# Performance work log

Measured on AMD Instinct MI355X. Metric: run time of the kernel, lower is better.

Reference implementation:

```python
import jax, jax.numpy as jnp
import numpy as np

B, T, D_IN, H, BR, D_OUT = 256, 500, 700, 200, 2, 35
V_TH = 1.0


def setup_inputs() -> dict:
    key = jax.random.key(0)
    ks = jax.random.split(key, 7)
    x = jax.random.normal(ks[0], (B, T, D_IN), dtype=jnp.float32)
    W_in = jax.random.normal(ks[1], (H * BR, D_IN), dtype=jnp.float32) * (1.0 / np.sqrt(D_IN))
    b_in = jax.random.normal(ks[2], (H * BR,), dtype=jnp.float32) * 0.01
    # tau_n ~ U(0, 4) per branch per neuron (as in SimpleDH_LIF init)
    tau_n = jax.random.uniform(ks[3], (H, BR), dtype=jnp.float32, minval=0.0, maxval=4.0)
    tau_m = jnp.full((H,), 2.0, dtype=jnp.float32)  # torch init: tensor(2.0) per neuron
    W_out = jax.random.normal(ks[5], (D_OUT, H), dtype=jnp.float32) * (1.0 / np.sqrt(H))
    b_out = jax.random.normal(ks[6], (D_OUT,), dtype=jnp.float32) * 0.01
    return {"x": x, "W_in": W_in, "b_in": b_in, "tau_n": tau_n,
            "tau_m": tau_m, "W_out": W_out, "b_out": b_out}


def reference(x, W_in, b_in, tau_n, tau_m, W_out, b_out):
    b, t, _ = x.shape
    # Batched input projection for all timesteps at once: (B,T,H*BR) -> (T,B,H,BR)
    branch_in = jnp.einsum('bti,oi->bto', x, W_in) + b_in
    branch_in = branch_in.reshape(b, t, H, BR).transpose(1, 0, 2, 3)

    beta = jax.nn.sigmoid(tau_n)          # (H, BR) dendritic branch decay
    alpha = jax.nn.sigmoid(tau_m)         # (H,)   soma membrane decay

    def step(carry, inp_t):
        v, i_d, counts = carry            # v:(B,H) i_d:(B,H,BR) counts:(B,H)
        i_d = beta * i_d + (1.0 - beta) * inp_t
        i_total = i_d.sum(axis=-1)        # (B,H)
        v = alpha * v + (1.0 - alpha) * i_total
        spike = (v >= V_TH).astype(v.dtype)
        v = v - spike * V_TH
        return (v, i_d, counts + spike), None

    v0 = jnp.zeros((b, H), dtype=x.dtype)
    i0 = jnp.zeros((b, H, BR), dtype=x.dtype)
    c0 = jnp.zeros((b, H), dtype=x.dtype)
    (v, i_d, spike_counts), _ = jax.lax.scan(step, (v0, i0, c0), branch_in)

    return spike_counts @ W_out.T + b_out  # (B, D_OUT)
```

## Files before the change

### kernel.cpp

```cpp
#include <hip/hip_runtime.h>

#define B_   256
#define T_   500
#define DIN  700
#define KP   704
#define H_   200
#define NO   400
#define DOUT 35
#define NKC  22

typedef _Float16 half_t;
typedef __attribute__((ext_vector_type(8))) _Float16 half8;
typedef __attribute__((ext_vector_type(4))) float floatx4;

#define SX 16.0f
#define SW 4096.0f
#define INV_S (1.0f / 65536.0f)

__device__ __forceinline__ float sigmoidf_(float x) {
    return 1.0f / (1.0f + expf(-x));
}

__global__ __launch_bounds__(256) void cvt_wfrag(
    const float* __restrict__ W, half_t* __restrict__ Whf, half_t* __restrict__ Wlf)
{
    int t = blockIdx.x * 256 + threadIdx.x;
    if (t >= NKC * 25 * 64) return;
    int lane = t & 63;
    int rest = t >> 6;
    int nfg  = rest % 25;
    int kc   = rest / 25;
    int la = lane & 15, lb = lane >> 4;
    int row = nfg * 16 + la;
    int col = kc * 32 + lb * 8;
    half8 hh, ll;
    #pragma unroll
    for (int j = 0; j < 8; ++j) {
        float v = (col + j < DIN) ? W[(size_t)row * DIN + col + j] : 0.0f;
        float s = v * SW;
        half_t h = (half_t)s;
        hh[j] = h;
        ll[j] = (half_t)(s - (float)h);
    }
    *reinterpret_cast<half8*>(&Whf[(size_t)t * 8]) = hh;
    *reinterpret_cast<half8*>(&Wlf[(size_t)t * 8]) = ll;
}

__global__ __launch_bounds__(256, 2) void dh_gemm_nolds(
    const float* __restrict__ x,
    const half_t* __restrict__ Whf, const half_t* __restrict__ Wlf,
    const float* __restrict__ bin, float* __restrict__ Y)
{
    int p = blockIdx.x;
    int xcd = p & 7, slot = p >> 3;
    int L = (xcd < 4 ? xcd * 313 : 4 * 313 + (xcd - 4) * 312) + slot;

    const int w    = threadIdx.x >> 6;
    const int lane = threadIdx.x & 63;
    const int la   = lane & 15;
    const int lb   = lane >> 4;

    const int wave = L * 4 + w;
    const int mt = wave / 5, nt = wave - mt * 5;
    const int m0 = mt * 64;
    const int o0 = nt * 80;

    floatx4 acc[4][5];
    #pragma unroll
    for (int mf = 0; mf < 4; ++mf)
        #pragma unroll
        for (int nf = 0; nf < 5; ++nf) {
            floatx4 z = {0.f, 0.f, 0.f, 0.f};
            acc[mf][nf] = z;
        }

    size_t arow[4];
    #pragma unroll
    for (int mf = 0; mf < 4; ++mf)
        arow[mf] = (size_t)(m0 + mf * 16 + la) * DIN;
    const size_t bbase = ((size_t)(nt * 5) * 64 + lane) * 8;

    float4 ra0[4][2], ra1[4][2];
    half8 b0h[5], b0l[5], b1h[5], b1l[5];
    half8 ah[4], al[4];

    auto LOADA = [&](float4 (&ra)[4][2], int kc) {
        const int col = kc * 32 + lb * 8;
        const int c2ofs = (col + 8 <= DIN) ? 4 : (692 - col);
        #pragma unroll
        for (int mf = 0; mf < 4; ++mf) {
            const float* ptr = &x[arow[mf] + col];
            ra[mf][0] = *reinterpret_cast<const float4*>(ptr);
            ra[mf][1] = *reinterpret_cast<const float4*>(ptr + c2ofs);
        }
    };
    auto LOADB = [&](half8 (&bh)[5], half8 (&bl)[5], int kc) {
        const size_t kofs = (size_t)kc * 25 * 64 * 8;
        #pragma unroll
        for (int nf = 0; nf < 5; ++nf) {
            size_t idx = bbase + kofs + (size_t)nf * 64 * 8;
            bh[nf] = *reinterpret_cast<const half8*>(&Whf[idx]);
            bl[nf] = *reinterpret_cast<const half8*>(&Wlf[idx]);
        }
    };
    auto CONV = [&](const float4 (&ra)[4][2]) {
        #pragma unroll
        for (int mf = 0; mf < 4; ++mf) {
            float vv[8];
            *reinterpret_cast<float4*>(&vv[0]) = ra[mf][0];
            *reinterpret_cast<float4*>(&vv[4]) = ra[mf][1];
            half8 hh, ll;
            #pragma unroll
            for (int j = 0; j < 8; ++j) {
                float s = vv[j] * SX;
                half_t h = (half_t)s;
                hh[j] = h;
                ll[j] = (half_t)(s - (float)h);
            }
            ah[mf] = hh;
            al[mf] = ll;
        }
    };
    auto MFMAS = [&](const half8 (&bh)[5], const half8 (&bl)[5]) {
        #pragma unroll
        for (int mf = 0; mf < 4; ++mf)
            #pragma unroll
            for (int nf = 0; nf < 5; ++nf)
                acc[mf][nf] = __builtin_amdgcn_mfma_f32_16x16x32_f16(ah[mf], bh[nf], acc[mf][nf], 0, 0, 0);
        #pragma unroll
        for (int mf = 0; mf < 4; ++mf)
            #pragma unroll
            for (int nf = 0; nf < 5; ++nf)
                acc[mf][nf] = __builtin_amdgcn_mfma_f32_16x16x32_f16(ah[mf], bl[nf], acc[mf][nf], 0, 0, 0);
        #pragma unroll
        for (int mf = 0; mf < 4; ++mf)
            #pragma unroll
            for (int nf = 0; nf < 5; ++nf)
                acc[mf][nf] = __builtin_amdgcn_mfma_f32_16x16x32_f16(al[mf], bh[nf], acc[mf][nf], 0, 0, 0);
    };

    LOADA(ra0, 0);
    LOADB(b0h, b0l, 0);
    #pragma unroll 1
    for (int kc2 = 0; kc2 < NKC; kc2 += 2) {
        LOADA(ra1, kc2 + 1);
        LOADB(b1h, b1l, kc2 + 1);
        CONV(ra0);
        MFMAS(b0h, b0l);
        if (kc2 + 2 < NKC) {
            LOADA(ra0, kc2 + 2);
            LOADB(b0h, b0l, kc2 + 2);
        }
        CONV(ra1);
        MFMAS(b1h, b1l);
    }

    float bo[5];
    #pragma unroll
    for (int nf = 0; nf < 5; ++nf) bo[nf] = bin[o0 + nf * 16 + la];

    #pragma unroll
    for (int mf = 0; mf < 4; ++mf) {
        int mbase = m0 + mf * 16 + lb * 4;
        #pragma unroll
        for (int rg = 0; rg < 4; ++rg) {
            int mm = mbase + rg;
            int bb = mm / T_;
            int tt = mm - bb * T_;
            float* yrow = &Y[((size_t)tt * B_ + bb) * NO + o0 + la];
            #pragma unroll
            for (int nf = 0; nf < 5; ++nf)
                yrow[nf * 16] = acc[mf][nf][rg] * INV_S + bo[nf];
        }
    }
}

#define BM 256
#define BN 64
#define BK 16
__global__ __launch_bounds__(256) void dh_gemm_in(
    const float* __restrict__ x, const float* __restrict__ Wt,
    const float* __restrict__ bin, float* __restrict__ Y)
{
    __shared__ float As[BK][BM + 4];
    __shared__ float Bs[BK][BN + 4];
    const int tid = threadIdx.x;
    const int tx = tid & 7;
    const int ty = tid >> 3;
    const int m0 = blockIdx.y * BM;
    const int o0 = blockIdx.x * BN;

    float acc[8][8];
    #pragma unroll
    for (int r = 0; r < 8; ++r)
        #pragma unroll
        for (int c = 0; c < 8; ++c) acc[r][c] = 0.0f;

    const int srow = tid >> 2;
    const int skq  = (tid & 3) << 2;

    for (int k0 = 0; k0 < DIN; k0 += BK) {
        float4 areg[4];
        #pragma unroll
        for (int i = 0; i < 4; ++i) {
            int idx = tid + i * 256;
            int row = idx >> 2;
            int kq  = (idx & 3) << 2;
            int kg  = k0 + kq;
            if (kg < DIN)
                areg[i] = *reinterpret_cast<const float4*>(&x[(size_t)(m0 + row) * DIN + kg]);
            else
                areg[i] = make_float4(0.f, 0.f, 0.f, 0.f);
        }
        float4 breg;
        {
            int kg = k0 + skq;
            int o  = o0 + srow;
            if (kg < DIN && o < NO)
                breg = *reinterpret_cast<const float4*>(&Wt[(size_t)o * DIN + kg]);
            else
                breg = make_float4(0.f, 0.f, 0.f, 0.f);
        }
        __syncthreads();
        #pragma unroll
        for (int i = 0; i < 4; ++i) {
            int idx = tid + i * 256;
            int row = idx >> 2;
            int kq  = (idx & 3) << 2;
            As[kq + 0][row] = areg[i].x;
            As[kq + 1][row] = areg[i].y;
            As[kq + 2][row] = areg[i].z;
            As[kq + 3][row] = areg[i].w;
        }
        Bs[skq + 0][srow] = breg.x;
        Bs[skq + 1][srow] = breg.y;
        Bs[skq + 2][srow] = breg.z;
        Bs[skq + 3][srow] = breg.w;
        __syncthreads();

        #pragma unroll
        for (int k = 0; k < BK; ++k) {
            float a[8], bb[8];
            *reinterpret_cast<float4*>(&a[0])  = *reinterpret_cast<const float4*>(&As[k][ty * 8]);
            *reinterpret_cast<float4*>(&a[4])  = *reinterpret_cast<const float4*>(&As[k][ty * 8 + 4]);
            *reinterpret_cast<float4*>(&bb[0]) = *reinterpret_cast<const float4*>(&Bs[k][tx * 8]);
            *reinterpret_cast<float4*>(&bb[4]) = *reinterpret_cast<const float4*>(&Bs[k][tx * 8 + 4]);
            #pragma unroll
            for (int r = 0; r < 8; ++r)
                #pragma unroll
                for (int c = 0; c < 8; ++c)
                    acc[r][c] = fmaf(a[r], bb[c], acc[r][c]);
        }
    }

    float bo[8];
    #pragma unroll
    for (int c = 0; c < 8; ++c) {
        int o = o0 + tx * 8 + c;
        bo[c] = (o < NO) ? bin[o] : 0.0f;
    }
    const int ob = o0 + tx * 8;
    if (ob < NO) {
        #pragma unroll
        for (int r = 0; r < 8; ++r) {
            int m = m0 + ty * 8 + r;
            int b = m / T_;
            int t = m - b * T_;
            float* yrow = &Y[((size_t)t * B_ + b) * NO];
            float4 v0 = make_float4(acc[r][0] + bo[0], acc[r][1] + bo[1],
                                    acc[r][2] + bo[2], acc[r][3] + bo[3]);
            float4 v1 = make_float4(acc[r][4] + bo[4], acc[r][5] + bo[5],
                                    acc[r][6] + bo[6], acc[r][7] + bo[7]);
            *reinterpret_cast<float4*>(&yrow[ob])     = v0;
            *reinterpret_cast<float4*>(&yrow[ob + 4]) = v1;
        }
    }
}

__global__ __launch_bounds__(64) void dh_scan(
    const float* __restrict__ Y, const float* __restrict__ tau_n,
    const float* __restrict__ tau_m, float* __restrict__ counts)
{
    int g = blockIdx.x * 64 + threadIdx.x;
    int b = g / H_;
    int h = g - b * H_;
    (void)b;
    float beta0 = sigmoidf_(tau_n[h * 2 + 0]);
    float beta1 = sigmoidf_(tau_n[h * 2 + 1]);
    float alpha = sigmoidf_(tau_m[h]);
    float omb0 = 1.0f - beta0, omb1 = 1.0f - beta1, oma = 1.0f - alpha;
    const float2* Yp = reinterpret_cast<const float2*>(Y);

    float v = 0.f, i0 = 0.f, i1 = 0.f, cnt = 0.f;
    #pragma unroll 1
    for (int t0 = 0; t0 < T_; t0 += 10) {
        float2 yb[10];
        #pragma unroll
        for (int j = 0; j < 10; ++j)
            yb[j] = Yp[(size_t)(t0 + j) * (B_ * H_) + g];
        #pragma unroll
        for (int j = 0; j < 10; ++j) {
            i0 = beta0 * i0 + omb0 * yb[j].x;
            i1 = beta1 * i1 + omb1 * yb[j].y;
            float it = i0 + i1;
            v = alpha * v + oma * it;
            if (v >= 1.0f) { v -= 1.0f; cnt += 1.0f; }
        }
    }
    counts[g] = cnt;
}

__global__ __launch_bounds__(64) void dh_out(
    const float* __restrict__ counts, const float* __restrict__ W_out,
    const float* __restrict__ b_out, float* __restrict__ out)
{
    int b = blockIdx.x;
    int o = threadIdx.x;
    if (o >= DOUT) return;
    float acc = b_out[o];
    const float* c = &counts[(size_t)b * H_];
    const float* w = &W_out[(size_t)o * H_];
    #pragma unroll 4
    for (int h = 0; h < H_; ++h)
        acc = fmaf(c[h], w[h], acc);
    out[(size_t)b * DOUT + o] = acc;
}

extern "C" void kernel_launch(void* const* d_in, const int* in_sizes, int n_in,
                              void* d_out, int out_size, void* d_ws, size_t ws_size,
                              hipStream_t stream) {
    const float* x     = (const float*)d_in[0];
    const float* W_in  = (const float*)d_in[1];
    const float* b_in  = (const float*)d_in[2];
    const float* tau_n = (const float*)d_in[3];
    const float* tau_m = (const float*)d_in[4];
    const float* W_out = (const float*)d_in[5];
    const float* b_out = (const float*)d_in[6];
    float* out = (float*)d_out;

    float* Y      = (float*)d_ws;
    float* counts = Y + (size_t)T_ * B_ * NO;

    const size_t nfrag_halves = (size_t)NKC * 25 * 64 * 8;
    size_t need = ((size_t)T_ * B_ * NO + (size_t)B_ * H_) * 4
                + 2 * nfrag_halves * 2;

    if (ws_size >= need) {
        half_t* Whf = (half_t*)(counts + (size_t)B_ * H_);
        half_t* Wlf = Whf + nfrag_halves;

        cvt_wfrag<<<(NKC * 25 * 64 + 255) / 256, 256, 0, stream>>>(W_in, Whf, Wlf);
        dh_gemm_nolds<<<2500, 256, 0, stream>>>(x, Whf, Wlf, b_in, Y);
    } else {
        dim3 g1(7, 500);
        dh_gemm_in<<<g1, 256, 0, stream>>>(x, W_in, b_in, Y);
    }

    dh_scan<<<(B_ * H_) / 64, 64, 0, stream>>>(Y, tau_n, tau_m, counts);
    dh_out<<<B_, 64, 0, stream>>>(counts, W_out, b_out, out);
}
```

Before: 413.1 us.

## Stage input GEMM A-tiles into LDS via direct global-to-LDS loads

Replaces per-lane strided float4 register loads of x with global_load_lds 16-byte transfers into a double-buffered, XOR-swizzled 64KB LDS tile. Each block now covers 256 rows by 80 outputs, and each wave stages and reads only its own 64 rows. Explicit vmcnt waits with sched_barriers overlap the next chunk's loads with compute. The aim is better coalescing of x reads and lower register pressure. The large LDS footprint limits occupancy to about two blocks per CU.

```diff
diff --git a/kernel.cpp b/kernel.cpp
--- a/kernel.cpp
+++ b/kernel.cpp
@@ -19,6 +19,13 @@
 
 __device__ __forceinline__ float sigmoidf_(float x) {
     return 1.0f / (1.0f + expf(-x));
+}
+
+__device__ __forceinline__ void gload_lds16(const float* g, float* l) {
+    __builtin_amdgcn_global_load_lds(
+        (const __attribute__((address_space(1))) unsigned int*)g,
+        (__attribute__((address_space(3))) unsigned int*)l,
+        16, 0, 0);
 }
 
 __global__ __launch_bounds__(256) void cvt_wfrag(
@@ -46,25 +53,24 @@
     *reinterpret_cast<half8*>(&Wlf[(size_t)t * 8]) = ll;
 }
 
-__global__ __launch_bounds__(256, 2) void dh_gemm_nolds(
+__global__ __launch_bounds__(256, 2) void dh_gemm_dma(
     const float* __restrict__ x,
     const half_t* __restrict__ Whf, const half_t* __restrict__ Wlf,
     const float* __restrict__ bin, float* __restrict__ Y)
 {
+    __shared__ float Abuf[2][8192];
+
     int p = blockIdx.x;
     int xcd = p & 7, slot = p >> 3;
     int L = (xcd < 4 ? xcd * 313 : 4 * 313 + (xcd - 4) * 312) + slot;
+    int by = L / 5, bx = L - by * 5;
+    const int m0 = by * 256, o0 = bx * 80;
 
     const int w    = threadIdx.x >> 6;
     const int lane = threadIdx.x & 63;
     const int la   = lane & 15;
     const int lb   = lane >> 4;
 
-    const int wave = L * 4 + w;
-    const int mt = wave / 5, nt = wave - mt * 5;
-    const int m0 = mt * 64;
-    const int o0 = nt * 80;
-
     floatx4 acc[4][5];
     #pragma unroll
     for (int mf = 0; mf < 4; ++mf)
@@ -74,24 +80,22 @@
             acc[mf][nf] = z;
         }
 
-    size_t arow[4];
-    #pragma unroll
-    for (int mf = 0; mf < 4; ++mf)
-        arow[mf] = (size_t)(m0 + mf * 16 + la) * DIN;
-    const size_t bbase = ((size_t)(nt * 5) * 64 + lane) * 8;
-
-    float4 ra0[4][2], ra1[4][2];
+    const size_t bbase = ((size_t)(bx * 5) * 64 + lane) * 8;
+
     half8 b0h[5], b0l[5], b1h[5], b1l[5];
     half8 ah[4], al[4];
 
-    auto LOADA = [&](float4 (&ra)[4][2], int kc) {
-        const int col = kc * 32 + lb * 8;
-        const int c2ofs = (col + 8 <= DIN) ? 4 : (692 - col);
-        #pragma unroll
-        for (int mf = 0; mf < 4; ++mf) {
-            const float* ptr = &x[arow[mf] + col];
-            ra[mf][0] = *reinterpret_cast<const float4*>(ptr);
-            ra[mf][1] = *reinterpret_cast<const float4*>(ptr + c2ofs);
+    const int wr8 = (lane >> 3);
+    const int wsp = (lane & 7) ^ (wr8 & 7);
+    auto STAGE = [&](int buf, int kc) {
+        #pragma unroll
+        for (int i = 0; i < 8; ++i) {
+            int r = (w * 8 + i) * 8 + wr8;
+            int col = kc * 32 + wsp * 4;
+            if (col >= DIN) col = 672;
+            const float* src = &x[(size_t)(m0 + r) * DIN + col];
+            float* dst = &Abuf[buf][(w * 8 + i) * 256];
+            gload_lds16(src, dst);
         }
     };
     auto LOADB = [&](half8 (&bh)[5], half8 (&bl)[5], int kc) {
@@ -103,12 +107,21 @@
             bl[nf] = *reinterpret_cast<const half8*>(&Wlf[idx]);
         }
     };
-    auto CONV = [&](const float4 (&ra)[4][2]) {
+    const int s0 = ((lb * 2)     ^ (la & 7)) * 4;
+    const int s1 = ((lb * 2 + 1) ^ (la & 7)) * 4;
+    auto COMPUTE = [&](const float* buf, const half8 (&bh)[5], const half8 (&bl)[5]) {
+        float4 f0[4], f1[4];
+        #pragma unroll
+        for (int mf = 0; mf < 4; ++mf) {
+            int rbase = (w * 64 + mf * 16 + la) * 32;
+            f0[mf] = *reinterpret_cast<const float4*>(&buf[rbase + s0]);
+            f1[mf] = *reinterpret_cast<const float4*>(&buf[rbase + s1]);
+        }
         #pragma unroll
         for (int mf = 0; mf < 4; ++mf) {
             float vv[8];
-            *reinterpret_cast<float4*>(&vv[0]) = ra[mf][0];
-            *reinterpret_cast<float4*>(&vv[4]) = ra[mf][1];
+            *reinterpret_cast<float4*>(&vv[0]) = f0[mf];
+            *reinterpret_cast<float4*>(&vv[4]) = f1[mf];
             half8 hh, ll;
             #pragma unroll
             for (int j = 0; j < 8; ++j) {
@@ -120,8 +133,6 @@
             ah[mf] = hh;
             al[mf] = ll;
         }
-    };
-    auto MFMAS = [&](const half8 (&bh)[5], const half8 (&bl)[5]) {
         #pragma unroll
         for (int mf = 0; mf < 4; ++mf)
             #pragma unroll
@@ -139,20 +150,30 @@
                 acc[mf][nf] = __builtin_amdgcn_mfma_f32_16x16x32_f16(al[mf], bh[nf], acc[mf][nf], 0, 0, 0);
     };
 
-    LOADA(ra0, 0);
+    STAGE(0, 0);
     LOADB(b0h, b0l, 0);
+
     #pragma unroll 1
     for (int kc2 = 0; kc2 < NKC; kc2 += 2) {
-        LOADA(ra1, kc2 + 1);
+        STAGE(1, kc2 + 1);
         LOADB(b1h, b1l, kc2 + 1);
-        CONV(ra0);
-        MFMAS(b0h, b0l);
+        __builtin_amdgcn_sched_barrier(0);
+        asm volatile("s_waitcnt vmcnt(18)" ::: "memory");
+        __builtin_amdgcn_sched_barrier(0);
+        COMPUTE(Abuf[0], b0h, b0l);
+
         if (kc2 + 2 < NKC) {
-            LOADA(ra0, kc2 + 2);
+            STAGE(0, kc2 + 2);
             LOADB(b0h, b0l, kc2 + 2);
-        }
-        CONV(ra1);
-        MFMAS(b1h, b1l);
+            __builtin_amdgcn_sched_barrier(0);
+            asm volatile("s_waitcnt vmcnt(18)" ::: "memory");
+            __builtin_amdgcn_sched_barrier(0);
+        } else {
+            __builtin_amdgcn_sched_barrier(0);
+            asm volatile("s_waitcnt vmcnt(0)" ::: "memory");
+            __builtin_amdgcn_sched_barrier(0);
+        }
+        COMPUTE(Abuf[1], b1h, b1l);
     }
 
     float bo[5];
@@ -161,7 +182,7 @@
 
     #pragma unroll
     for (int mf = 0; mf < 4; ++mf) {
-        int mbase = m0 + mf * 16 + lb * 4;
+        int mbase = m0 + w * 64 + mf * 16 + lb * 4;
         #pragma unroll
         for (int rg = 0; rg < 4; ++rg) {
             int mm = mbase + rg;
@@ -350,7 +371,7 @@
         half_t* Wlf = Whf + nfrag_halves;
 
         cvt_wfrag<<<(NKC * 25 * 64 + 255) / 256, 256, 0, stream>>>(W_in, Whf, Wlf);
-        dh_gemm_nolds<<<2500, 256, 0, stream>>>(x, Whf, Wlf, b_in, Y);
+        dh_gemm_dma<<<2500, 256, 0, stream>>>(x, Whf, Wlf, b_in, Y);
     } else {
         dim3 g1(7, 500);
         dh_gemm_in<<<g1, 256, 0, stream>>>(x, W_in, b_in, Y);
```

New measurement: 478.7 us. 1.16x slower.

## Shrink per-wave GEMM tile to 32 rows and raise occupancy

Applied to the files above, without the earlier changes.

The split-fp16 input-projection GEMM now gives each wave a 32x80 output tile instead of 64x80. All four waves in a block share the same N tile across 128 consecutive rows, and the launch doubles to 5000 blocks with an occupancy hint of 3 blocks per CU. B-fragment loads are no longer double-buffered; they are issued inside each compute step. The aim is to cut register pressure so more waves hide memory latency, at the cost of reloading B fragments twice as often and losing B prefetch overlap.

```diff
diff --git a/kernel.cpp b/kernel.cpp
--- a/kernel.cpp
+++ b/kernel.cpp
@@ -46,55 +46,53 @@
     *reinterpret_cast<half8*>(&Wlf[(size_t)t * 8]) = ll;
 }
 
-__global__ __launch_bounds__(256, 2) void dh_gemm_nolds(
+__global__ __launch_bounds__(256, 3) void dh_gemm_w32(
     const float* __restrict__ x,
     const half_t* __restrict__ Whf, const half_t* __restrict__ Wlf,
     const float* __restrict__ bin, float* __restrict__ Y)
 {
     int p = blockIdx.x;
-    int xcd = p & 7, slot = p >> 3;
-    int L = (xcd < 4 ? xcd * 313 : 4 * 313 + (xcd - 4) * 312) + slot;
+    int L = (p & 7) * 625 + (p >> 3);
+    int by = L / 5, bx = L - by * 5;
 
     const int w    = threadIdx.x >> 6;
     const int lane = threadIdx.x & 63;
     const int la   = lane & 15;
     const int lb   = lane >> 4;
 
-    const int wave = L * 4 + w;
-    const int mt = wave / 5, nt = wave - mt * 5;
-    const int m0 = mt * 64;
-    const int o0 = nt * 80;
-
-    floatx4 acc[4][5];
-    #pragma unroll
-    for (int mf = 0; mf < 4; ++mf)
+    const int m0 = by * 128 + w * 32;
+    const int o0 = bx * 80;
+
+    floatx4 acc[2][5];
+    #pragma unroll
+    for (int mf = 0; mf < 2; ++mf)
         #pragma unroll
         for (int nf = 0; nf < 5; ++nf) {
             floatx4 z = {0.f, 0.f, 0.f, 0.f};
             acc[mf][nf] = z;
         }
 
-    size_t arow[4];
-    #pragma unroll
-    for (int mf = 0; mf < 4; ++mf)
+    size_t arow[2];
+    #pragma unroll
+    for (int mf = 0; mf < 2; ++mf)
         arow[mf] = (size_t)(m0 + mf * 16 + la) * DIN;
-    const size_t bbase = ((size_t)(nt * 5) * 64 + lane) * 8;
-
-    float4 ra0[4][2], ra1[4][2];
-    half8 b0h[5], b0l[5], b1h[5], b1l[5];
-    half8 ah[4], al[4];
-
-    auto LOADA = [&](float4 (&ra)[4][2], int kc) {
+    const size_t bbase = ((size_t)(bx * 5) * 64 + lane) * 8;
+
+    float4 raA[2][2], raB[2][2];
+
+    auto LOADA = [&](float4 (&ra)[2][2], int kc) {
         const int col = kc * 32 + lb * 8;
         const int c2ofs = (col + 8 <= DIN) ? 4 : (692 - col);
         #pragma unroll
-        for (int mf = 0; mf < 4; ++mf) {
+        for (int mf = 0; mf < 2; ++mf) {
             const float* ptr = &x[arow[mf] + col];
             ra[mf][0] = *reinterpret_cast<const float4*>(ptr);
             ra[mf][1] = *reinterpret_cast<const float4*>(ptr + c2ofs);
         }
     };
-    auto LOADB = [&](half8 (&bh)[5], half8 (&bl)[5], int kc) {
+
+    auto COMPUTE = [&](const float4 (&ra)[2][2], int kc) {
+        half8 bh[5], bl[5];
         const size_t kofs = (size_t)kc * 25 * 64 * 8;
         #pragma unroll
         for (int nf = 0; nf < 5; ++nf) {
@@ -102,10 +100,9 @@
             bh[nf] = *reinterpret_cast<const half8*>(&Whf[idx]);
             bl[nf] = *reinterpret_cast<const half8*>(&Wlf[idx]);
         }
-    };
-    auto CONV = [&](const float4 (&ra)[4][2]) {
-        #pragma unroll
-        for (int mf = 0; mf < 4; ++mf) {
+        half8 ah[2], al[2];
+        #pragma unroll
+        for (int mf = 0; mf < 2; ++mf) {
             float vv[8];
             *reinterpret_cast<float4*>(&vv[0]) = ra[mf][0];
             *reinterpret_cast<float4*>(&vv[4]) = ra[mf][1];
@@ -120,39 +117,30 @@
             ah[mf] = hh;
             al[mf] = ll;
         }
-    };
-    auto MFMAS = [&](const half8 (&bh)[5], const half8 (&bl)[5]) {
-        #pragma unroll
-        for (int mf = 0; mf < 4; ++mf)
+        #pragma unroll
+        for (int mf = 0; mf < 2; ++mf)
             #pragma unroll
             for (int nf = 0; nf < 5; ++nf)
                 acc[mf][nf] = __builtin_amdgcn_mfma_f32_16x16x32_f16(ah[mf], bh[nf], acc[mf][nf], 0, 0, 0);
         #pragma unroll
-        for (int mf = 0; mf < 4; ++mf)
+        for (int mf = 0; mf < 2; ++mf)
             #pragma unroll
             for (int nf = 0; nf < 5; ++nf)
                 acc[mf][nf] = __builtin_amdgcn_mfma_f32_16x16x32_f16(ah[mf], bl[nf], acc[mf][nf], 0, 0, 0);
         #pragma unroll
-        for (int mf = 0; mf < 4; ++mf)
+        for (int mf = 0; mf < 2; ++mf)
             #pragma unroll
             for (int nf = 0; nf < 5; ++nf)
                 acc[mf][nf] = __builtin_amdgcn_mfma_f32_16x16x32_f16(al[mf], bh[nf], acc[mf][nf], 0, 0, 0);
     };
 
-    LOADA(ra0, 0);
-    LOADB(b0h, b0l, 0);
+    LOADA(raA, 0);
     #pragma unroll 1
-    for (int kc2 = 0; kc2 < NKC; kc2 += 2) {
-        LOADA(ra1, kc2 + 1);
-        LOADB(b1h, b1l, kc2 + 1);
-        CONV(ra0);
-        MFMAS(b0h, b0l);
-        if (kc2 + 2 < NKC) {
-            LOADA(ra0, kc2 + 2);
-            LOADB(b0h, b0l, kc2 + 2);
-        }
-        CONV(ra1);
-        MFMAS(b1h, b1l);
+    for (int kc = 0; kc < NKC; kc += 2) {
+        LOADA(raB, kc + 1);
+        COMPUTE(raA, kc);
+        if (kc + 2 < NKC) LOADA(raA, kc + 2);
+        COMPUTE(raB, kc + 1);
     }
 
     float bo[5];
@@ -160,7 +148,7 @@
     for (int nf = 0; nf < 5; ++nf) bo[nf] = bin[o0 + nf * 16 + la];
 
     #pragma unroll
-    for (int mf = 0; mf < 4; ++mf) {
+    for (int mf = 0; mf < 2; ++mf) {
         int mbase = m0 + mf * 16 + lb * 4;
         #pragma unroll
         for (int rg = 0; rg < 4; ++rg) {
@@ -350,7 +338,7 @@
         half_t* Wlf = Whf + nfrag_halves;
 
         cvt_wfrag<<<(NKC * 25 * 64 + 255) / 256, 256, 0, stream>>>(W_in, Whf, Wlf);
-        dh_gemm_nolds<<<2500, 256, 0, stream>>>(x, Whf, Wlf, b_in, Y);
+        dh_gemm_w32<<<5000, 256, 0, stream>>>(x, Whf, Wlf, b_in, Y);
     } else {
         dim3 g1(7, 500);
         dh_gemm_in<<<g1, 256, 0, stream>>>(x, W_in, b_in, Y);
```

Result: slower. 440.0 us (+6.5%).

## Software-pipeline GEMM so fp16 conversion overlaps MFMAs, with sched barriers

Applied to the files above, without the earlier changes.

Restructures the input-projection GEMM main loop into a deeper software pipeline. It double-buffers the converted fp16 hi/lo A fragments so the conversion of the next K chunk can be issued alongside the current chunk's MFMAs. Loads run two chunks ahead, and sched_barrier calls pin the instruction order. Occupancy is lowered from two blocks per CU to one to give room for the extra registers, which risks less latency hiding across waves. Out-of-range prefetches are clamped to the last chunk.

```diff
diff --git a/kernel.cpp b/kernel.cpp
--- a/kernel.cpp
+++ b/kernel.cpp
@@ -3,7 +3,6 @@
 #define B_   256
 #define T_   500
 #define DIN  700
-#define KP   704
 #define H_   200
 #define NO   400
 #define DOUT 35
@@ -46,7 +45,7 @@
     *reinterpret_cast<half8*>(&Wlf[(size_t)t * 8]) = ll;
 }
 
-__global__ __launch_bounds__(256, 2) void dh_gemm_nolds(
+__global__ __launch_bounds__(256, 1) void dh_gemm_ovl(
     const float* __restrict__ x,
     const half_t* __restrict__ Whf, const half_t* __restrict__ Wlf,
     const float* __restrict__ bin, float* __restrict__ Y)
@@ -80,11 +79,12 @@
         arow[mf] = (size_t)(m0 + mf * 16 + la) * DIN;
     const size_t bbase = ((size_t)(nt * 5) * 64 + lane) * 8;
 
-    float4 ra0[4][2], ra1[4][2];
-    half8 b0h[5], b0l[5], b1h[5], b1l[5];
-    half8 ah[4], al[4];
+    float4 aE[4][2], aO[4][2];
+    half8 bEh[5], bEl[5], bOh[5], bOl[5];
+    half8 fEh[4], fEl[4], fOh[4], fOl[4];
 
     auto LOADA = [&](float4 (&ra)[4][2], int kc) {
+        if (kc > NKC - 1) kc = NKC - 1;
         const int col = kc * 32 + lb * 8;
         const int c2ofs = (col + 8 <= DIN) ? 4 : (692 - col);
         #pragma unroll
@@ -95,6 +95,7 @@
         }
     };
     auto LOADB = [&](half8 (&bh)[5], half8 (&bl)[5], int kc) {
+        if (kc > NKC - 1) kc = NKC - 1;
         const size_t kofs = (size_t)kc * 25 * 64 * 8;
         #pragma unroll
         for (int nf = 0; nf < 5; ++nf) {
@@ -103,7 +104,7 @@
             bl[nf] = *reinterpret_cast<const half8*>(&Wlf[idx]);
         }
     };
-    auto CONV = [&](const float4 (&ra)[4][2]) {
+    auto CONV = [&](half8 (&fh)[4], half8 (&fl)[4], const float4 (&ra)[4][2]) {
         #pragma unroll
         for (int mf = 0; mf < 4; ++mf) {
             float vv[8];
@@ -117,43 +118,58 @@
                 hh[j] = h;
                 ll[j] = (half_t)(s - (float)h);
             }
-            ah[mf] = hh;
-            al[mf] = ll;
+            fh[mf] = hh;
+            fl[mf] = ll;
         }
     };
-    auto MFMAS = [&](const half8 (&bh)[5], const half8 (&bl)[5]) {
+    auto MFMAS = [&](const half8 (&fh)[4], const half8 (&fl)[4],
+                     const half8 (&bh)[5], const half8 (&bl)[5]) {
         #pragma unroll
         for (int mf = 0; mf < 4; ++mf)
             #pragma unroll
             for (int nf = 0; nf < 5; ++nf)
-                acc[mf][nf] = __builtin_amdgcn_mfma_f32_16x16x32_f16(ah[mf], bh[nf], acc[mf][nf], 0, 0, 0);
+                acc[mf][nf] = __builtin_amdgcn_mfma_f32_16x16x32_f16(fh[mf], bh[nf], acc[mf][nf], 0, 0, 0);
         #pragma unroll
         for (int mf = 0; mf < 4; ++mf)
             #pragma unroll
             for (int nf = 0; nf < 5; ++nf)
-                acc[mf][nf] = __builtin_amdgcn_mfma_f32_16x16x32_f16(ah[mf], bl[nf], acc[mf][nf], 0, 0, 0);
+                acc[mf][nf] = __builtin_amdgcn_mfma_f32_16x16x32_f16(fh[mf], bl[nf], acc[mf][nf], 0, 0, 0);
         #pragma unroll
         for (int mf = 0; mf < 4; ++mf)
             #pragma unroll
             for (int nf = 0; nf < 5; ++nf)
-                acc[mf][nf] = __builtin_amdgcn_mfma_f32_16x16x32_f16(al[mf], bh[nf], acc[mf][nf], 0, 0, 0);
+                acc[mf][nf] = __builtin_amdgcn_mfma_f32_16x16x32_f16(fl[mf], bh[nf], acc[mf][nf], 0, 0, 0);
     };
 
-    LOADA(ra0, 0);
-    LOADB(b0h, b0l, 0);
+#define SBAR() __builtin_amdgcn_sched_barrier(0)
+
+    LOADA(aE, 0); SBAR();
+    LOADB(bEh, bEl, 0); SBAR();
+    LOADA(aO, 1); SBAR();
+    LOADB(bOh, bOl, 1); SBAR();
+    CONV(fEh, fEl, aE);
+    SBAR();
+    LOADA(aE, 2);
+    SBAR();
+
     #pragma unroll 1
-    for (int kc2 = 0; kc2 < NKC; kc2 += 2) {
-        LOADA(ra1, kc2 + 1);
-        LOADB(b1h, b1l, kc2 + 1);
-        CONV(ra0);
-        MFMAS(b0h, b0l);
-        if (kc2 + 2 < NKC) {
-            LOADA(ra0, kc2 + 2);
-            LOADB(b0h, b0l, kc2 + 2);
-        }
-        CONV(ra1);
-        MFMAS(b1h, b1l);
-    }
+    for (int I = 0; I < 10; ++I) {
+        const int kc = 2 * I;
+        MFMAS(fEh, fEl, bEh, bEl);
+        CONV(fOh, fOl, aO);
+        SBAR();
+        LOADB(bEh, bEl, kc + 2); SBAR();
+        LOADA(aO, kc + 3); SBAR();
+        MFMAS(fOh, fOl, bOh, bOl);
+        CONV(fEh, fEl, aE);
+        SBAR();
+        LOADB(bOh, bOl, kc + 3); SBAR();
+        LOADA(aE, kc + 4); SBAR();
+    }
+    MFMAS(fEh, fEl, bEh, bEl);
+    CONV(fOh, fOl, aO);
+    SBAR();
+    MFMAS(fOh, fOl, bOh, bOl);
 
     float bo[5];
     #pragma unroll
@@ -173,6 +189,7 @@
                 yrow[nf * 16] = acc[mf][nf][rg] * INV_S + bo[nf];
         }
     }
+#undef SBAR
 }
 
 #define BM 256
@@ -350,7 +367,7 @@
         half_t* Wlf = Whf + nfrag_halves;
 
         cvt_wfrag<<<(NKC * 25 * 64 + 255) / 256, 256, 0, stream>>>(W_in, Whf, Wlf);
-        dh_gemm_nolds<<<2500, 256, 0, stream>>>(x, Whf, Wlf, b_in, Y);
+        dh_gemm_ovl<<<2500, 256, 0, stream>>>(x, Whf, Wlf, b_in, Y);
     } else {
         dim3 g1(7, 500);
         dh_gemm_in<<<g1, 256, 0, stream>>>(x, W_in, b_in, Y);
```

Measured after the change: 396.8 us. -4.0%, faster.
